# Optimization experiments

Measured on AMD Instinct MI355X. Metric: run time of the kernel, lower is better.

Reference implementation:

```python
import jax, jax.numpy as jnp
import numpy as np

N, F_IN, PRE, K = 400000, 64, 32, 6
EDGE = [32, 32]


def _dense_params(key, fan_in, fan_out):
    kw, kb = jax.random.split(key)
    W = jax.random.normal(kw, (fan_in, fan_out), jnp.float32) / np.sqrt(fan_in).astype(np.float32)
    b = jnp.zeros((fan_out,), jnp.float32)
    return W, b


def setup_inputs() -> dict:
    key = jax.random.key(0)
    ks = jax.random.split(key, 10)
    x = jax.random.normal(ks[0], (N, F_IN), jnp.float32)
    distsq = jax.random.uniform(ks[1], (N, K), jnp.float32)
    nidx = jax.random.randint(ks[2], (N, K), 0, N, jnp.int64)
    Wp, bp = _dense_params(ks[3], F_IN, PRE)
    # edge MLP: input K*(PRE+1) -> 32 -> 32 -> K
    We1, be1 = _dense_params(ks[4], K * (PRE + 1), EDGE[0])
    We2, be2 = _dense_params(ks[5], EDGE[0], EDGE[1])
    We3, be3 = _dense_params(ks[6], EDGE[1], K)
    # self MLP: F_IN -> 32 -> 32 -> 1
    Ws1, bs1 = _dense_params(ks[7], F_IN, EDGE[0])
    Ws2, bs2 = _dense_params(ks[8], EDGE[0], EDGE[1])
    Ws3, bs3 = _dense_params(ks[9], EDGE[1], 1)
    return dict(x=x, distsq=distsq, nidx=nidx, Wp=Wp, bp=bp,
                We1=We1, be1=be1, We2=We2, be2=be2, We3=We3, be3=be3,
                Ws1=Ws1, bs1=bs1, Ws2=Ws2, bs2=bs2, Ws3=Ws3, bs3=bs3)


def _forward(x, distsq, nidx, Wp, bp, We1, be1, We2, be2, We3, be3,
             Ws1, bs1, Ws2, bs2, Ws3, bs3):
    # pre-dense: [N, PRE]
    x_p = jax.nn.elu(x @ Wp + bp)
    # gather neighbors; select(nidx, x_n, 0.0) masks nidx<0 to 0.0
    safe_idx = jnp.maximum(nidx, 0)
    gathered = x_p[safe_idx]                              # [N, K, PRE]
    gathered = jnp.where(nidx[:, :, None] < 0, 0.0, gathered)
    diff = x_p[:, None, :] - gathered                     # [N, K, PRE]
    xn = jnp.concatenate([diff, distsq[:, :, None]], axis=2)  # [N, K, PRE+1]
    xn = xn.reshape(xn.shape[0], K * (PRE + 1))
    xn = jax.nn.elu(xn @ We1 + be1)
    xn = jax.nn.elu(xn @ We2 + be2)
    xn = xn @ We3 + be3                                   # [N, K]
    xs = jax.nn.elu(x @ Ws1 + bs1)
    xs = jax.nn.elu(xs @ Ws2 + bs2)
    xs = xs @ Ws3 + bs3                                   # [N, 1]
    out = jnp.concatenate([xs, xn], axis=1)               # [N, K+1]
    return jax.nn.softmax(out, axis=1)


def reference(x, distsq, nidx, Wp, bp, We1, be1, We2, be2, We3, be3,
              Ws1, bs1, Ws2, bs2, Ws3, bs3):
    return _forward(x, distsq, nidx, Wp, bp, We1, be1, We2, be2, We3, be3,
                    Ws1, bs1, Ws2, bs2, Ws3, bs3)
```

## Files before the change

kernel.cpp:

```cpp
#include <hip/hip_runtime.h>
#include <hip/hip_bf16.h>
#include <math.h>

typedef __hip_bfloat16 bf16;
typedef __attribute__((ext_vector_type(8))) __bf16 bf16x8;
typedef __attribute__((ext_vector_type(4))) float f32x4;

#define F_IN 64
#define KNB 6

#define WOFF_WP   0
#define WOFF_BP   2048
#define WOFF_WE1  2080
#define WOFF_BE1  8416
#define WOFF_WE2  8448
#define WOFF_BE2  9472
#define WOFF_WE3  9504
#define WOFF_BE3  9696
#define WOFF_WS1  9728
#define WOFF_BS1  11776
#define WOFF_WS2  11808
#define WOFF_BS2  12832
#define WOFF_WS3  12864
#define WOFF_BS3  12896
#define FLAGS_OFF 13056
#define WOFF_WSUM 13312
#define WOFF_WDSQ 14336
#define STAGE_OFF 16384

__device__ __forceinline__ float b2f(bf16 v) { return __bfloat162float(v); }
__device__ __forceinline__ float eluf(float v) { return v > 0.f ? v : expm1f(v); }

__device__ __forceinline__ ushort f2bu(float v) {
  __bf16 b = (__bf16)v; ushort u; __builtin_memcpy(&u, &b, 2); return u;
}

union U8 { uint4 u; bf16x8 v; ushort s[8]; };

__device__ __forceinline__ void lds_fence() {
  __builtin_amdgcn_wave_barrier();
  __builtin_amdgcn_s_waitcnt(0xC07F);
  __builtin_amdgcn_wave_barrier();
}

__global__ void detect(const ushort* xb, const int* ni, int* flags) {
  if (threadIdx.x == 0 && blockIdx.x == 0) {
    int bad = 0;
    for (int i = 0; i < 256; i++) {
      float v = __uint_as_float(((unsigned)xb[i]) << 16);
      if (!(fabsf(v) < 100.f)) bad++;
    }
    int hi_nonzero = 0;
    for (int i = 0; i < 64; i++) if (ni[2 * i + 1] != 0) hi_nonzero = 1;
    flags[0] = (bad < 8) ? 1 : 0;
    flags[1] = hi_nonzero ? 0 : 1;
  }
}

__global__ void wstage(const void* Wp, const void* bp, const void* We1, const void* be1,
                       const void* We2, const void* be2, const void* We3, const void* be3,
                       const void* Ws1, const void* bs1, const void* Ws2, const void* bs2,
                       const void* Ws3, const void* bs3, float* w, const int* flags) {
  const void* srcs[14] = {Wp, bp, We1, be1, We2, be2, We3, be3, Ws1, bs1, Ws2, bs2, Ws3, bs3};
  const int sizes[14] = {2048, 32, 6336, 32, 1024, 32, 192, 6, 2048, 32, 1024, 32, 32, 1};
  const int offs[14] = {WOFF_WP, WOFF_BP, WOFF_WE1, WOFF_BE1, WOFF_WE2, WOFF_BE2, WOFF_WE3,
                        WOFF_BE3, WOFF_WS1, WOFF_BS1, WOFF_WS2, WOFF_BS2, WOFF_WS3, WOFF_BS3};
  int bf = flags[0];
  int t = blockIdx.x;
  const void* s = srcs[t];
  int nel = sizes[t];
  float* d = w + offs[t];
  if (bf) {
    const bf16* sb = (const bf16*)s;
    for (int i = threadIdx.x; i < nel; i += blockDim.x) d[i] = b2f(sb[i]);
  } else {
    const float* sf = (const float*)s;
    for (int i = threadIdx.x; i < nel; i += blockDim.x) d[i] = sf[i];
  }
}

__global__ void wprep(float* w) {
  int t = blockIdx.x * blockDim.x + threadIdx.x;
  if (t < 1024) {
    int j = t >> 5, o = t & 31;
    float s = 0.f;
    for (int k = 0; k < KNB; k++) s += w[WOFF_WE1 + (k * 33 + j) * 32 + o];
    w[WOFF_WSUM + t] = s;
  }
  if (t < 192) {
    int k = t >> 5, o = t & 31;
    w[WOFF_WDSQ + t] = w[WOFF_WE1 + (k * 33 + 32) * 32 + o];
  }
}

__device__ __forceinline__ bf16x8 bfrag(const float* W, int ld, int nValid, int kValid, float sgn) {
  int lane = threadIdx.x & 63;
  int n = lane & 15, quad = lane >> 4;
  bf16x8 r;
#pragma unroll
  for (int j = 0; j < 8; j++) {
    int k = quad * 8 + j;
    float v = (n < nValid && k < kValid) ? sgn * W[k * ld + n] : 0.f;
    r[j] = (__bf16)v;
  }
  return r;
}

template <bool BF16>
__device__ __forceinline__ bf16x8 afrag_row(const void* base, long row, int k0) {
  int quad = (threadIdx.x & 63) >> 4;
  if (BF16) {
    U8 u;
    u.u = *(const uint4*)((const ushort*)base + row * F_IN + k0 + quad * 8);
    return u.v;
  } else {
    const float* p = (const float*)base + row * F_IN + k0 + quad * 8;
    float4 a = *(const float4*)p, b = *(const float4*)(p + 4);
    bf16x8 r;
    r[0] = (__bf16)a.x; r[1] = (__bf16)a.y; r[2] = (__bf16)a.z; r[3] = (__bf16)a.w;
    r[4] = (__bf16)b.x; r[5] = (__bf16)b.y; r[6] = (__bf16)b.z; r[7] = (__bf16)b.w;
    return r;
  }
}

template <bool BF16>
__device__ void pre_tiles(const void* xv, const float* __restrict__ w,
                          ushort* __restrict__ xp, float* __restrict__ xs,
                          int n_nodes, ushort* buf) {
  int lane = threadIdx.x & 63;
  int m = lane & 15, quad = lane >> 4;

  bf16x8 fwp[2][2], fws1[2][2], fws2[2], fws3;
#pragma unroll
  for (int s = 0; s < 2; s++)
#pragma unroll
    for (int t = 0; t < 2; t++) {
      fwp[s][t]  = bfrag(w + WOFF_WP  + s * 32 * 32 + 16 * t, 32, 16, 32, 1.f);
      fws1[s][t] = bfrag(w + WOFF_WS1 + s * 32 * 32 + 16 * t, 32, 16, 32, 1.f);
    }
#pragma unroll
  for (int t = 0; t < 2; t++) fws2[t] = bfrag(w + WOFF_WS2 + 16 * t, 32, 16, 32, 1.f);
  fws3 = bfrag(w + WOFF_WS3, 1, 1, 32, 1.f);
  float bpv[2], bs1v[2], bs2v[2];
#pragma unroll
  for (int t = 0; t < 2; t++) {
    bpv[t]  = w[WOFF_BP  + m + 16 * t];
    bs1v[t] = w[WOFF_BS1 + m + 16 * t];
    bs2v[t] = w[WOFF_BS2 + m + 16 * t];
  }
  float bs3f = w[WOFF_BS3];

  int T = (n_nodes + 15) >> 4;
  int wid = (int)((blockIdx.x * blockDim.x + threadIdx.x) >> 6);
  int nw = (int)((gridDim.x * blockDim.x) >> 6);
  f32x4 zero = {0.f, 0.f, 0.f, 0.f};

  for (int t0 = wid; t0 < T; t0 += nw) {
    long n0 = (long)t0 * 16;
    long row = n0 + m; if (row >= n_nodes) row = n_nodes - 1;
    bf16x8 a0 = afrag_row<BF16>(xv, row, 0);
    bf16x8 a1 = afrag_row<BF16>(xv, row, 32);
    f32x4 accp[2], accs[2];
#pragma unroll
    for (int t = 0; t < 2; t++) {
      accp[t] = __builtin_amdgcn_mfma_f32_16x16x32_bf16(a0, fwp[0][t], zero, 0, 0, 0);
      accp[t] = __builtin_amdgcn_mfma_f32_16x16x32_bf16(a1, fwp[1][t], accp[t], 0, 0, 0);
      accs[t] = __builtin_amdgcn_mfma_f32_16x16x32_bf16(a0, fws1[0][t], zero, 0, 0, 0);
      accs[t] = __builtin_amdgcn_mfma_f32_16x16x32_bf16(a1, fws1[1][t], accs[t], 0, 0, 0);
    }
#pragma unroll
    for (int t = 0; t < 2; t++)
#pragma unroll
      for (int r = 0; r < 4; r++)
        buf[(quad * 4 + r) * 32 + m + 16 * t] = f2bu(eluf(accp[t][r] + bpv[t]));
    lds_fence();
    {
      uint4 rv = *(const uint4*)(buf + m * 32 + quad * 8);
      *(uint4*)(xp + row * 32 + quad * 8) = rv;
    }
#pragma unroll
    for (int t = 0; t < 2; t++)
#pragma unroll
      for (int r = 0; r < 4; r++)
        buf[(quad * 4 + r) * 32 + m + 16 * t] = f2bu(eluf(accs[t][r] + bs1v[t]));
    lds_fence();
    U8 as1; as1.u = *(const uint4*)(buf + m * 32 + quad * 8);
    f32x4 acc2[2];
#pragma unroll
    for (int t = 0; t < 2; t++)
      acc2[t] = __builtin_amdgcn_mfma_f32_16x16x32_bf16(as1.v, fws2[t], zero, 0, 0, 0);
#pragma unroll
    for (int t = 0; t < 2; t++)
#pragma unroll
      for (int r = 0; r < 4; r++)
        buf[(quad * 4 + r) * 32 + m + 16 * t] = f2bu(eluf(acc2[t][r] + bs2v[t]));
    lds_fence();
    U8 as2; as2.u = *(const uint4*)(buf + m * 32 + quad * 8);
    f32x4 accx = __builtin_amdgcn_mfma_f32_16x16x32_bf16(as2.v, fws3, zero, 0, 0, 0);
    if (m == 0) {
#pragma unroll
      for (int r = 0; r < 4; r++) {
        long orow = n0 + quad * 4 + r;
        if (orow < n_nodes) xs[orow] = accx[r] + bs3f;
      }
    }
    lds_fence();
  }
}

__launch_bounds__(256)
__global__ void preK(const void* xv, const float* __restrict__ w,
                     const int* __restrict__ flags,
                     ushort* __restrict__ xp, float* __restrict__ xs, int n_nodes) {
  __shared__ ushort sb[4 * 512];
  ushort* buf = sb + (threadIdx.x >> 6) * 512;
  if (flags[0]) pre_tiles<true>(xv, w, xp, xs, n_nodes, buf);
  else          pre_tiles<false>(xv, w, xp, xs, n_nodes, buf);
}

template <bool BF16>
__device__ void edge_tiles(const ushort* __restrict__ xp, const float* __restrict__ xs,
                           const void* dsv, const int* __restrict__ ni, int i64,
                           const float* __restrict__ w, void* outv, int n_nodes,
                           ushort* buf, float* lbuf) {
  int lane = threadIdx.x & 63;
  int m = lane & 15, quad = lane >> 4;

  bf16x8 fsum[2], fwe1[KNB][2], fdsq[2], fwe2[2], fwe3;
#pragma unroll
  for (int t = 0; t < 2; t++) {
    fsum[t] = bfrag(w + WOFF_WSUM + 16 * t, 32, 16, 32, 1.f);
    fdsq[t] = bfrag(w + WOFF_WDSQ + 16 * t, 32, 16, KNB, 1.f);
    fwe2[t] = bfrag(w + WOFF_WE2 + 16 * t, 32, 16, 32, 1.f);
#pragma unroll
    for (int k = 0; k < KNB; k++)
      fwe1[k][t] = bfrag(w + WOFF_WE1 + k * 33 * 32 + 16 * t, 32, 16, 32, -1.f);
  }
  fwe3 = bfrag(w + WOFF_WE3, 6, 6, 32, 1.f);
  float be1v[2], be2v[2];
#pragma unroll
  for (int t = 0; t < 2; t++) {
    be1v[t] = w[WOFF_BE1 + m + 16 * t];
    be2v[t] = w[WOFF_BE2 + m + 16 * t];
  }
  float be3v = (m < 6) ? w[WOFF_BE3 + m] : 0.f;

  int T = (n_nodes + 15) >> 4;
  int wid = (int)((blockIdx.x * blockDim.x + threadIdx.x) >> 6);
  int nw = (int)((gridDim.x * blockDim.x) >> 6);
  f32x4 zero = {0.f, 0.f, 0.f, 0.f};

  for (int t0 = wid; t0 < T; t0 += nw) {
    long n0 = (long)t0 * 16;
    long row = n0 + m; if (row >= n_nodes) row = n_nodes - 1;

    int idxs[KNB];
#pragma unroll
    for (int k = 0; k < KNB; k++)
      idxs[k] = i64 ? ni[(row * KNB + k) * 2] : ni[row * KNB + k];

    U8 own; own.u = *(const uint4*)(xp + row * 32 + quad * 8);
    U8 nb[KNB];
#pragma unroll
    for (int k = 0; k < KNB; k++) {
      long ai = idxs[k];
      if (ai < 0 || ai >= n_nodes) ai = 0;
      nb[k].u = *(const uint4*)(xp + ai * 32 + quad * 8);
      if (idxs[k] < 0) { nb[k].u.x = 0; nb[k].u.y = 0; nb[k].u.z = 0; nb[k].u.w = 0; }
    }

    U8 ad; ad.u.x = 0; ad.u.y = 0; ad.u.z = 0; ad.u.w = 0;
    if (quad == 0) {
      if (BF16) {
        const unsigned* dp = (const unsigned*)dsv;
        ad.u.x = dp[row * 3 + 0];
        ad.u.y = dp[row * 3 + 1];
        ad.u.z = dp[row * 3 + 2];
      } else {
        const float* dp = (const float*)dsv + row * KNB;
#pragma unroll
        for (int k = 0; k < KNB; k++) ad.s[k] = f2bu(dp[k]);
      }
    }

    f32x4 accA[2], accB[2];
#pragma unroll
    for (int t = 0; t < 2; t++) {
      accA[t] = __builtin_amdgcn_mfma_f32_16x16x32_bf16(own.v, fsum[t], zero, 0, 0, 0);
      accA[t] = __builtin_amdgcn_mfma_f32_16x16x32_bf16(nb[0].v, fwe1[0][t], accA[t], 0, 0, 0);
      accA[t] = __builtin_amdgcn_mfma_f32_16x16x32_bf16(nb[1].v, fwe1[1][t], accA[t], 0, 0, 0);
      accA[t] = __builtin_amdgcn_mfma_f32_16x16x32_bf16(nb[2].v, fwe1[2][t], accA[t], 0, 0, 0);
      accB[t] = __builtin_amdgcn_mfma_f32_16x16x32_bf16(nb[3].v, fwe1[3][t], zero, 0, 0, 0);
      accB[t] = __builtin_amdgcn_mfma_f32_16x16x32_bf16(nb[4].v, fwe1[4][t], accB[t], 0, 0, 0);
      accB[t] = __builtin_amdgcn_mfma_f32_16x16x32_bf16(nb[5].v, fwe1[5][t], accB[t], 0, 0, 0);
      accB[t] = __builtin_amdgcn_mfma_f32_16x16x32_bf16(ad.v, fdsq[t], accB[t], 0, 0, 0);
    }
#pragma unroll
    for (int t = 0; t < 2; t++)
#pragma unroll
      for (int r = 0; r < 4; r++)
        buf[(quad * 4 + r) * 32 + m + 16 * t] =
            f2bu(eluf(accA[t][r] + accB[t][r] + be1v[t]));
    lds_fence();
    U8 a1; a1.u = *(const uint4*)(buf + m * 32 + quad * 8);
    f32x4 acc2[2];
#pragma unroll
    for (int t = 0; t < 2; t++)
      acc2[t] = __builtin_amdgcn_mfma_f32_16x16x32_bf16(a1.v, fwe2[t], zero, 0, 0, 0);
#pragma unroll
    for (int t = 0; t < 2; t++)
#pragma unroll
      for (int r = 0; r < 4; r++)
        buf[(quad * 4 + r) * 32 + m + 16 * t] = f2bu(eluf(acc2[t][r] + be2v[t]));
    lds_fence();
    U8 a2; a2.u = *(const uint4*)(buf + m * 32 + quad * 8);
    f32x4 acc3 = __builtin_amdgcn_mfma_f32_16x16x32_bf16(a2.v, fwe3, zero, 0, 0, 0);

    if (m < 6) {
#pragma unroll
      for (int r = 0; r < 4; r++) lbuf[(quad * 4 + r) * 8 + m] = acc3[r] + be3v;
    }
    lds_fence();
    if (lane < 16) {
      long nodeid = n0 + lane;
      if (nodeid < n_nodes) {
        float lg[7];
        lg[0] = xs[nodeid];
#pragma unroll
        for (int i = 0; i < 6; i++) lg[1 + i] = lbuf[lane * 8 + i];
        float mx = lg[0];
#pragma unroll
        for (int i = 1; i < 7; i++) mx = fmaxf(mx, lg[i]);
        float e[7], ssum = 0.f;
#pragma unroll
        for (int i = 0; i < 7; i++) { e[i] = expf(lg[i] - mx); ssum += e[i]; }
        float inv = 1.f / ssum;
        if (BF16) {
          ushort* o = (ushort*)outv + nodeid * 7;
#pragma unroll
          for (int i = 0; i < 7; i++) o[i] = f2bu(e[i] * inv);
        } else {
          float* o = (float*)outv + nodeid * 7;
#pragma unroll
          for (int i = 0; i < 7; i++) o[i] = e[i] * inv;
        }
      }
    }
    lds_fence();
  }
}

__launch_bounds__(256)
__global__ void edgeK(const ushort* __restrict__ xp, const float* __restrict__ xs,
                      const void* dsv, const int* __restrict__ ni,
                      const float* __restrict__ w, const int* __restrict__ flags,
                      void* outv, int n_nodes) {
  __shared__ ushort sb[4 * 512];
  __shared__ float sl[4 * 128];
  ushort* buf = sb + (threadIdx.x >> 6) * 512;
  float* lbuf = sl + (threadIdx.x >> 6) * 128;
  int bf = flags[0];
  int i64 = flags[1];
  if (bf) edge_tiles<true>(xp, xs, dsv, ni, i64, w, outv, n_nodes, buf, lbuf);
  else    edge_tiles<false>(xp, xs, dsv, ni, i64, w, outv, n_nodes, buf, lbuf);
}

__device__ __forceinline__ void bf8_to_f32(uint4 u, float* f) {
  unsigned int w[4] = {u.x, u.y, u.z, u.w};
#pragma unroll
  for (int i = 0; i < 4; i++) {
    f[2 * i]     = __uint_as_float(w[i] << 16);
    f[2 * i + 1] = __uint_as_float(w[i] & 0xffff0000u);
  }
}

template <bool BF16>
__device__ __forceinline__ void load_row8(const void* base, long row, int chunk, float* f) {
  if (BF16) {
    const uint4* p = (const uint4*)((const ushort*)base + row * F_IN);
    bf8_to_f32(p[chunk], f);
  } else {
    const float4* p = (const float4*)((const float*)base + row * F_IN);
    float4 a = p[2 * chunk];
    float4 b = p[2 * chunk + 1];
    f[0] = a.x; f[1] = a.y; f[2] = a.z; f[3] = a.w;
    f[4] = b.x; f[5] = b.y; f[6] = b.z; f[7] = b.w;
  }
}

template <bool BF16>
__device__ void node_body(int n, int n_nodes, const void* xv, const void* dsv,
                          const int* __restrict__ ni, int i64,
                          const float* __restrict__ w, void* outv) {
  const float* Wp  = w + WOFF_WP;
  const float* bp  = w + WOFF_BP;
  const float* We1 = w + WOFF_WE1;
  const float* be1 = w + WOFF_BE1;
  const float* We2 = w + WOFF_WE2;
  const float* be2 = w + WOFF_BE2;
  const float* We3 = w + WOFF_WE3;
  const float* be3 = w + WOFF_BE3;
  const float* Ws1 = w + WOFF_WS1;
  const float* bs1 = w + WOFF_BS1;
  const float* Ws2 = w + WOFF_WS2;
  const float* bs2 = w + WOFF_BS2;
  const float* Ws3 = w + WOFF_WS3;
  const float* bs3 = w + WOFF_BS3;

  float h[32], s1[32];
#pragma unroll
  for (int o = 0; o < 32; o++) { h[o] = bp[o]; s1[o] = bs1[o]; }
  for (int c = 0; c < 8; c++) {
    float xv8[8];
    load_row8<BF16>(xv, n, c, xv8);
#pragma unroll
    for (int q = 0; q < 8; q++) {
      int j = c * 8 + q;
      float xj = xv8[q];
#pragma unroll
      for (int o = 0; o < 32; o++) {
        h[o]  += xj * Wp[j * 32 + o];
        s1[o] += xj * Ws1[j * 32 + o];
      }
    }
  }
  float own[32];
#pragma unroll
  for (int o = 0; o < 32; o++) own[o] = eluf(h[o]);
  float s2[32];
#pragma unroll
  for (int o = 0; o < 32; o++) s2[o] = bs2[o];
  for (int j = 0; j < 32; j++) {
    float v = eluf(s1[j]);
#pragma unroll
    for (int o = 0; o < 32; o++) s2[o] += v * Ws2[j * 32 + o];
  }
  float xsv = bs3[0];
#pragma unroll
  for (int j = 0; j < 32; j++) xsv += eluf(s2[j]) * Ws3[j];

  float h1[32];
#pragma unroll
  for (int o = 0; o < 32; o++) h1[o] = be1[o];
  for (int k = 0; k < KNB; k++) {
    long pos = (long)n * KNB + k;
    int idx = i64 ? ni[2 * pos] : ni[pos];
    float mmask = idx < 0 ? 0.f : 1.f;
    long ai = idx < 0 ? 0 : idx;
    if (ai >= n_nodes) ai = 0;
    float nh[32];
#pragma unroll
    for (int o = 0; o < 32; o++) nh[o] = bp[o];
    for (int c = 0; c < 8; c++) {
      float xv8[8];
      load_row8<BF16>(xv, ai, c, xv8);
#pragma unroll
      for (int q = 0; q < 8; q++) {
        int j = c * 8 + q;
        float xj = xv8[q];
#pragma unroll
        for (int o = 0; o < 32; o++) nh[o] += xj * Wp[j * 32 + o];
      }
    }
    const float* Wk = We1 + (k * 33) * 32;
#pragma unroll
    for (int j = 0; j < 32; j++) {
      float d = own[j] - mmask * eluf(nh[j]);
#pragma unroll
      for (int o = 0; o < 32; o++) h1[o] += d * Wk[j * 32 + o];
    }
    float dsq = BF16 ? b2f(((const bf16*)dsv)[pos]) : ((const float*)dsv)[pos];
#pragma unroll
    for (int o = 0; o < 32; o++) h1[o] += dsq * Wk[32 * 32 + o];
  }
  float h2[32];
#pragma unroll
  for (int o = 0; o < 32; o++) h2[o] = be2[o];
  for (int j = 0; j < 32; j++) {
    float v = eluf(h1[j]);
#pragma unroll
    for (int o = 0; o < 32; o++) h2[o] += v * We2[j * 32 + o];
  }
  float lg[7];
  lg[0] = xsv;
#pragma unroll
  for (int o = 0; o < 6; o++) lg[1 + o] = be3[o];
  for (int j = 0; j < 32; j++) {
    float v = eluf(h2[j]);
#pragma unroll
    for (int o = 0; o < 6; o++) lg[1 + o] += v * We3[j * 6 + o];
  }
  float mx = lg[0];
#pragma unroll
  for (int i = 1; i < 7; i++) mx = fmaxf(mx, lg[i]);
  float e[7], ssum = 0.f;
#pragma unroll
  for (int i = 0; i < 7; i++) { e[i] = expf(lg[i] - mx); ssum += e[i]; }
  float inv = 1.f / ssum;
  if (BF16) {
    bf16* o = (bf16*)outv;
#pragma unroll
    for (int i = 0; i < 7; i++) o[(long)n * 7 + i] = __float2bfloat16(e[i] * inv);
  } else {
    float* o = (float*)outv;
#pragma unroll
    for (int i = 0; i < 7; i++) o[(long)n * 7 + i] = e[i] * inv;
  }
}

__launch_bounds__(256)
__global__ void fused(const void* xv, const void* dsv, const int* __restrict__ ni,
                      const float* __restrict__ w, const int* __restrict__ flags,
                      void* outv, int n_nodes) {
  int n = blockIdx.x * blockDim.x + threadIdx.x;
  if (n >= n_nodes) return;
  int bf = flags[0];
  int i64 = flags[1];
  if (bf) node_body<true>(n, n_nodes, xv, dsv, ni, i64, w, outv);
  else    node_body<false>(n, n_nodes, xv, dsv, ni, i64, w, outv);
}

extern "C" void kernel_launch(void* const* d_in, const int* in_sizes, int n_in,
                              void* d_out, int out_size, void* d_ws, size_t ws_size,
                              hipStream_t stream) {
  const void* x      = d_in[0];
  const void* distsq = d_in[1];
  const int*  nidx   = (const int*)d_in[2];

  float* w = (float*)d_ws;
  int* flags = (int*)(w + FLAGS_OFF);
  int n_nodes = in_sizes[0] / F_IN;

  detect<<<1, 64, 0, stream>>>((const ushort*)x, nidx, flags);
  wstage<<<14, 256, 0, stream>>>(d_in[3], d_in[4], d_in[5], d_in[6], d_in[7], d_in[8],
                                 d_in[9], d_in[10], d_in[11], d_in[12], d_in[13], d_in[14],
                                 d_in[15], d_in[16], w, flags);
  wprep<<<4, 256, 0, stream>>>(w);

  size_t need = (size_t)STAGE_OFF * 4 + (size_t)n_nodes * 64 + (size_t)n_nodes * 4 + 256;
  if (ws_size >= need) {
    ushort* xp = (ushort*)(w + STAGE_OFF);
    float* xs = (float*)(xp + (size_t)n_nodes * 32);
    preK<<<1024, 256, 0, stream>>>(x, w, flags, xp, xs, n_nodes);
    edgeK<<<1024, 256, 0, stream>>>(xp, xs, distsq, nidx, w, flags, d_out, n_nodes);
  } else {
    int grid = (n_nodes + 255) / 256;
    fused<<<grid, 256, 0, stream>>>(x, distsq, nidx, w, flags, d_out, n_nodes);
  }
}
```

Measured before the change: 298.9 us.

## Drop weight staging kernels; read weights directly and detect dtype per block

Removes the detect, wstage and wprep launches. Each block now computes the dtype and index-width flags itself with a ballot, and builds its MFMA weight fragments straight from the input tensors, summing We1 over neighbours in place. It also doubles the grid for the pre and edge kernels, switches exp to the fast __expf intrinsic, and reorders the MFMA chain so the own-feature term is accumulated last. This saves three small serialized launches at the cost of redundant per-block flag detection and fragment construction.

```diff
diff --git a/kernel.cpp b/kernel.cpp
--- a/kernel.cpp
+++ b/kernel.cpp
@@ -9,30 +9,17 @@
 #define F_IN 64
 #define KNB 6
 
-#define WOFF_WP   0
-#define WOFF_BP   2048
-#define WOFF_WE1  2080
-#define WOFF_BE1  8416
-#define WOFF_WE2  8448
-#define WOFF_BE2  9472
-#define WOFF_WE3  9504
-#define WOFF_BE3  9696
-#define WOFF_WS1  9728
-#define WOFF_BS1  11776
-#define WOFF_WS2  11808
-#define WOFF_BS2  12832
-#define WOFF_WS3  12864
-#define WOFF_BS3  12896
-#define FLAGS_OFF 13056
-#define WOFF_WSUM 13312
-#define WOFF_WDSQ 14336
-#define STAGE_OFF 16384
-
 __device__ __forceinline__ float b2f(bf16 v) { return __bfloat162float(v); }
-__device__ __forceinline__ float eluf(float v) { return v > 0.f ? v : expm1f(v); }
+__device__ __forceinline__ float eluf(float v) { return v > 0.f ? v : __expf(v) - 1.f; }
 
 __device__ __forceinline__ ushort f2bu(float v) {
   __bf16 b = (__bf16)v; ushort u; __builtin_memcpy(&u, &b, 2); return u;
+}
+
+template <bool BF16>
+__device__ __forceinline__ float wval(const void* W, long i) {
+  if (BF16) return b2f(((const bf16*)W)[i]);
+  return ((const float*)W)[i];
 }
 
 union U8 { uint4 u; bf16x8 v; ushort s[8]; };
@@ -43,65 +30,52 @@
   __builtin_amdgcn_wave_barrier();
 }
 
-__global__ void detect(const ushort* xb, const int* ni, int* flags) {
-  if (threadIdx.x == 0 && blockIdx.x == 0) {
+__device__ __forceinline__ void block_flags(const ushort* xb, const int* ni, int* sflags) {
+  if (threadIdx.x < 64) {
+    int t = threadIdx.x;
     int bad = 0;
-    for (int i = 0; i < 256; i++) {
+    for (int i = t; i < 256; i += 64) {
       float v = __uint_as_float(((unsigned)xb[i]) << 16);
       if (!(fabsf(v) < 100.f)) bad++;
     }
-    int hi_nonzero = 0;
-    for (int i = 0; i < 64; i++) if (ni[2 * i + 1] != 0) hi_nonzero = 1;
-    flags[0] = (bad < 8) ? 1 : 0;
-    flags[1] = hi_nonzero ? 0 : 1;
-  }
-}
-
-__global__ void wstage(const void* Wp, const void* bp, const void* We1, const void* be1,
-                       const void* We2, const void* be2, const void* We3, const void* be3,
-                       const void* Ws1, const void* bs1, const void* Ws2, const void* bs2,
-                       const void* Ws3, const void* bs3, float* w, const int* flags) {
-  const void* srcs[14] = {Wp, bp, We1, be1, We2, be2, We3, be3, Ws1, bs1, Ws2, bs2, Ws3, bs3};
-  const int sizes[14] = {2048, 32, 6336, 32, 1024, 32, 192, 6, 2048, 32, 1024, 32, 32, 1};
-  const int offs[14] = {WOFF_WP, WOFF_BP, WOFF_WE1, WOFF_BE1, WOFF_WE2, WOFF_BE2, WOFF_WE3,
-                        WOFF_BE3, WOFF_WS1, WOFF_BS1, WOFF_WS2, WOFF_BS2, WOFF_WS3, WOFF_BS3};
-  int bf = flags[0];
-  int t = blockIdx.x;
-  const void* s = srcs[t];
-  int nel = sizes[t];
-  float* d = w + offs[t];
-  if (bf) {
-    const bf16* sb = (const bf16*)s;
-    for (int i = threadIdx.x; i < nel; i += blockDim.x) d[i] = b2f(sb[i]);
-  } else {
-    const float* sf = (const float*)s;
-    for (int i = threadIdx.x; i < nel; i += blockDim.x) d[i] = sf[i];
-  }
-}
-
-__global__ void wprep(float* w) {
-  int t = blockIdx.x * blockDim.x + threadIdx.x;
-  if (t < 1024) {
-    int j = t >> 5, o = t & 31;
-    float s = 0.f;
-    for (int k = 0; k < KNB; k++) s += w[WOFF_WE1 + (k * 33 + j) * 32 + o];
-    w[WOFF_WSUM + t] = s;
-  }
-  if (t < 192) {
-    int k = t >> 5, o = t & 31;
-    w[WOFF_WDSQ + t] = w[WOFF_WE1 + (k * 33 + 32) * 32 + o];
-  }
-}
-
-__device__ __forceinline__ bf16x8 bfrag(const float* W, int ld, int nValid, int kValid, float sgn) {
+    unsigned long long bm = __ballot(bad > 0);
+    unsigned long long hm = __ballot(ni[2 * t + 1] != 0);
+    if (t == 0) {
+      sflags[0] = (__popcll(bm) < 4) ? 1 : 0;
+      sflags[1] = (hm == 0ULL) ? 1 : 0;
+    }
+  }
+  __syncthreads();
+}
+
+template <bool BF16>
+__device__ __forceinline__ bf16x8 bfragT(const void* W, long base, int ld,
+                                         int nValid, int kValid, float sgn) {
   int lane = threadIdx.x & 63;
   int n = lane & 15, quad = lane >> 4;
   bf16x8 r;
 #pragma unroll
   for (int j = 0; j < 8; j++) {
     int k = quad * 8 + j;
-    float v = (n < nValid && k < kValid) ? sgn * W[k * ld + n] : 0.f;
+    float v = (n < nValid && k < kValid) ? sgn * wval<BF16>(W, base + (long)k * ld + n) : 0.f;
     r[j] = (__bf16)v;
+  }
+  return r;
+}
+
+template <bool BF16>
+__device__ __forceinline__ bf16x8 fsum_frag(const void* We1, int t) {
+  int lane = threadIdx.x & 63;
+  int n = lane & 15, quad = lane >> 4;
+  bf16x8 r;
+#pragma unroll
+  for (int j = 0; j < 8; j++) {
+    int k = quad * 8 + j;
+    float s = 0.f;
+#pragma unroll
+    for (int kk = 0; kk < KNB; kk++)
+      s += wval<BF16>(We1, ((long)(kk * 33 + k)) * 32 + n + 16 * t);
+    r[j] = (__bf16)s;
   }
   return r;
 }
@@ -124,7 +98,9 @@
 }
 
 template <bool BF16>
-__device__ void pre_tiles(const void* xv, const float* __restrict__ w,
+__device__ void pre_tiles(const void* xv,
+                          const void* Wp, const void* bp, const void* Ws1, const void* bs1,
+                          const void* Ws2, const void* bs2, const void* Ws3, const void* bs3,
                           ushort* __restrict__ xp, float* __restrict__ xs,
                           int n_nodes, ushort* buf) {
   int lane = threadIdx.x & 63;
@@ -135,20 +111,20 @@
   for (int s = 0; s < 2; s++)
 #pragma unroll
     for (int t = 0; t < 2; t++) {
-      fwp[s][t]  = bfrag(w + WOFF_WP  + s * 32 * 32 + 16 * t, 32, 16, 32, 1.f);
-      fws1[s][t] = bfrag(w + WOFF_WS1 + s * 32 * 32 + 16 * t, 32, 16, 32, 1.f);
-    }
-#pragma unroll
-  for (int t = 0; t < 2; t++) fws2[t] = bfrag(w + WOFF_WS2 + 16 * t, 32, 16, 32, 1.f);
-  fws3 = bfrag(w + WOFF_WS3, 1, 1, 32, 1.f);
+      fwp[s][t]  = bfragT<BF16>(Wp,  s * 1024 + 16 * t, 32, 16, 32, 1.f);
+      fws1[s][t] = bfragT<BF16>(Ws1, s * 1024 + 16 * t, 32, 16, 32, 1.f);
+    }
+#pragma unroll
+  for (int t = 0; t < 2; t++) fws2[t] = bfragT<BF16>(Ws2, 16 * t, 32, 16, 32, 1.f);
+  fws3 = bfragT<BF16>(Ws3, 0, 1, 1, 32, 1.f);
   float bpv[2], bs1v[2], bs2v[2];
 #pragma unroll
   for (int t = 0; t < 2; t++) {
-    bpv[t]  = w[WOFF_BP  + m + 16 * t];
-    bs1v[t] = w[WOFF_BS1 + m + 16 * t];
-    bs2v[t] = w[WOFF_BS2 + m + 16 * t];
-  }
-  float bs3f = w[WOFF_BS3];
+    bpv[t]  = wval<BF16>(bp,  m + 16 * t);
+    bs1v[t] = wval<BF16>(bs1, m + 16 * t);
+    bs2v[t] = wval<BF16>(bs2, m + 16 * t);
+  }
+  float bs3f = wval<BF16>(bs3, 0);
 
   int T = (n_nodes + 15) >> 4;
   int wid = (int)((blockIdx.x * blockDim.x + threadIdx.x) >> 6);
@@ -208,42 +184,46 @@
   }
 }
 
-__launch_bounds__(256)
-__global__ void preK(const void* xv, const float* __restrict__ w,
-                     const int* __restrict__ flags,
+__launch_bounds__(256, 4)
+__global__ void preK(const void* xv, const int* ni,
+                     const void* Wp, const void* bp, const void* Ws1, const void* bs1,
+                     const void* Ws2, const void* bs2, const void* Ws3, const void* bs3,
                      ushort* __restrict__ xp, float* __restrict__ xs, int n_nodes) {
   __shared__ ushort sb[4 * 512];
+  __shared__ int sflags[2];
+  block_flags((const ushort*)xv, ni, sflags);
   ushort* buf = sb + (threadIdx.x >> 6) * 512;
-  if (flags[0]) pre_tiles<true>(xv, w, xp, xs, n_nodes, buf);
-  else          pre_tiles<false>(xv, w, xp, xs, n_nodes, buf);
+  if (sflags[0]) pre_tiles<true>(xv, Wp, bp, Ws1, bs1, Ws2, bs2, Ws3, bs3, xp, xs, n_nodes, buf);
+  else           pre_tiles<false>(xv, Wp, bp, Ws1, bs1, Ws2, bs2, Ws3, bs3, xp, xs, n_nodes, buf);
 }
 
 template <bool BF16>
 __device__ void edge_tiles(const ushort* __restrict__ xp, const float* __restrict__ xs,
                            const void* dsv, const int* __restrict__ ni, int i64,
-                           const float* __restrict__ w, void* outv, int n_nodes,
-                           ushort* buf, float* lbuf) {
+                           const void* We1, const void* be1, const void* We2, const void* be2,
+                           const void* We3, const void* be3,
+                           void* outv, int n_nodes, ushort* buf, float* lbuf) {
   int lane = threadIdx.x & 63;
   int m = lane & 15, quad = lane >> 4;
 
   bf16x8 fsum[2], fwe1[KNB][2], fdsq[2], fwe2[2], fwe3;
 #pragma unroll
   for (int t = 0; t < 2; t++) {
-    fsum[t] = bfrag(w + WOFF_WSUM + 16 * t, 32, 16, 32, 1.f);
-    fdsq[t] = bfrag(w + WOFF_WDSQ + 16 * t, 32, 16, KNB, 1.f);
-    fwe2[t] = bfrag(w + WOFF_WE2 + 16 * t, 32, 16, 32, 1.f);
+    fsum[t] = fsum_frag<BF16>(We1, t);
+    fdsq[t] = bfragT<BF16>(We1, 1024 + 16 * t, 1056, 16, KNB, 1.f);
+    fwe2[t] = bfragT<BF16>(We2, 16 * t, 32, 16, 32, 1.f);
 #pragma unroll
     for (int k = 0; k < KNB; k++)
-      fwe1[k][t] = bfrag(w + WOFF_WE1 + k * 33 * 32 + 16 * t, 32, 16, 32, -1.f);
-  }
-  fwe3 = bfrag(w + WOFF_WE3, 6, 6, 32, 1.f);
+      fwe1[k][t] = bfragT<BF16>(We1, (long)k * 1056 + 16 * t, 32, 16, 32, -1.f);
+  }
+  fwe3 = bfragT<BF16>(We3, 0, 6, 6, 32, 1.f);
   float be1v[2], be2v[2];
 #pragma unroll
   for (int t = 0; t < 2; t++) {
-    be1v[t] = w[WOFF_BE1 + m + 16 * t];
-    be2v[t] = w[WOFF_BE2 + m + 16 * t];
-  }
-  float be3v = (m < 6) ? w[WOFF_BE3 + m] : 0.f;
+    be1v[t] = wval<BF16>(be1, m + 16 * t);
+    be2v[t] = wval<BF16>(be2, m + 16 * t);
+  }
+  float be3v = (m < 6) ? wval<BF16>(be3, m) : 0.f;
 
   int T = (n_nodes + 15) >> 4;
   int wid = (int)((blockIdx.x * blockDim.x + threadIdx.x) >> 6);
@@ -282,19 +262,21 @@
         for (int k = 0; k < KNB; k++) ad.s[k] = f2bu(dp[k]);
       }
     }
+    float xsv = xs[row];
 
     f32x4 accA[2], accB[2];
 #pragma unroll
     for (int t = 0; t < 2; t++) {
-      accA[t] = __builtin_amdgcn_mfma_f32_16x16x32_bf16(own.v, fsum[t], zero, 0, 0, 0);
-      accA[t] = __builtin_amdgcn_mfma_f32_16x16x32_bf16(nb[0].v, fwe1[0][t], accA[t], 0, 0, 0);
+      accA[t] = __builtin_amdgcn_mfma_f32_16x16x32_bf16(nb[0].v, fwe1[0][t], zero, 0, 0, 0);
       accA[t] = __builtin_amdgcn_mfma_f32_16x16x32_bf16(nb[1].v, fwe1[1][t], accA[t], 0, 0, 0);
       accA[t] = __builtin_amdgcn_mfma_f32_16x16x32_bf16(nb[2].v, fwe1[2][t], accA[t], 0, 0, 0);
       accB[t] = __builtin_amdgcn_mfma_f32_16x16x32_bf16(nb[3].v, fwe1[3][t], zero, 0, 0, 0);
       accB[t] = __builtin_amdgcn_mfma_f32_16x16x32_bf16(nb[4].v, fwe1[4][t], accB[t], 0, 0, 0);
       accB[t] = __builtin_amdgcn_mfma_f32_16x16x32_bf16(nb[5].v, fwe1[5][t], accB[t], 0, 0, 0);
       accB[t] = __builtin_amdgcn_mfma_f32_16x16x32_bf16(ad.v, fdsq[t], accB[t], 0, 0, 0);
-    }
+      accA[t] = __builtin_amdgcn_mfma_f32_16x16x32_bf16(own.v, fsum[t], accA[t], 0, 0, 0);
+    }
+
 #pragma unroll
     for (int t = 0; t < 2; t++)
 #pragma unroll
@@ -333,7 +315,7 @@
         for (int i = 1; i < 7; i++) mx = fmaxf(mx, lg[i]);
         float e[7], ssum = 0.f;
 #pragma unroll
-        for (int i = 0; i < 7; i++) { e[i] = expf(lg[i] - mx); ssum += e[i]; }
+        for (int i = 0; i < 7; i++) { e[i] = __expf(lg[i] - mx); ssum += e[i]; }
         float inv = 1.f / ssum;
         if (BF16) {
           ushort* o = (ushort*)outv + nodeid * 7;
@@ -347,81 +329,44 @@
       }
     }
     lds_fence();
+    (void)xsv;
   }
 }
 
 __launch_bounds__(256)
 __global__ void edgeK(const ushort* __restrict__ xp, const float* __restrict__ xs,
                       const void* dsv, const int* __restrict__ ni,
-                      const float* __restrict__ w, const int* __restrict__ flags,
-                      void* outv, int n_nodes) {
+                      const void* We1, const void* be1, const void* We2, const void* be2,
+                      const void* We3, const void* be3,
+                      const void* xv_probe, void* outv, int n_nodes) {
   __shared__ ushort sb[4 * 512];
   __shared__ float sl[4 * 128];
+  __shared__ int sflags[2];
+  block_flags((const ushort*)xv_probe, ni, sflags);
   ushort* buf = sb + (threadIdx.x >> 6) * 512;
   float* lbuf = sl + (threadIdx.x >> 6) * 128;
-  int bf = flags[0];
-  int i64 = flags[1];
-  if (bf) edge_tiles<true>(xp, xs, dsv, ni, i64, w, outv, n_nodes, buf, lbuf);
-  else    edge_tiles<false>(xp, xs, dsv, ni, i64, w, outv, n_nodes, buf, lbuf);
-}
-
-__device__ __forceinline__ void bf8_to_f32(uint4 u, float* f) {
-  unsigned int w[4] = {u.x, u.y, u.z, u.w};
-#pragma unroll
-  for (int i = 0; i < 4; i++) {
-    f[2 * i]     = __uint_as_float(w[i] << 16);
-    f[2 * i + 1] = __uint_as_float(w[i] & 0xffff0000u);
-  }
-}
-
-template <bool BF16>
-__device__ __forceinline__ void load_row8(const void* base, long row, int chunk, float* f) {
-  if (BF16) {
-    const uint4* p = (const uint4*)((const ushort*)base + row * F_IN);
-    bf8_to_f32(p[chunk], f);
-  } else {
-    const float4* p = (const float4*)((const float*)base + row * F_IN);
-    float4 a = p[2 * chunk];
-    float4 b = p[2 * chunk + 1];
-    f[0] = a.x; f[1] = a.y; f[2] = a.z; f[3] = a.w;
-    f[4] = b.x; f[5] = b.y; f[6] = b.z; f[7] = b.w;
-  }
+  if (sflags[0]) edge_tiles<true>(xp, xs, dsv, ni, sflags[1], We1, be1, We2, be2, We3, be3,
+                                  outv, n_nodes, buf, lbuf);
+  else           edge_tiles<false>(xp, xs, dsv, ni, sflags[1], We1, be1, We2, be2, We3, be3,
+                                   outv, n_nodes, buf, lbuf);
 }
 
 template <bool BF16>
 __device__ void node_body(int n, int n_nodes, const void* xv, const void* dsv,
                           const int* __restrict__ ni, int i64,
-                          const float* __restrict__ w, void* outv) {
-  const float* Wp  = w + WOFF_WP;
-  const float* bp  = w + WOFF_BP;
-  const float* We1 = w + WOFF_WE1;
-  const float* be1 = w + WOFF_BE1;
-  const float* We2 = w + WOFF_WE2;
-  const float* be2 = w + WOFF_BE2;
-  const float* We3 = w + WOFF_WE3;
-  const float* be3 = w + WOFF_BE3;
-  const float* Ws1 = w + WOFF_WS1;
-  const float* bs1 = w + WOFF_BS1;
-  const float* Ws2 = w + WOFF_WS2;
-  const float* bs2 = w + WOFF_BS2;
-  const float* Ws3 = w + WOFF_WS3;
-  const float* bs3 = w + WOFF_BS3;
-
+                          const void* Wp, const void* bp, const void* We1, const void* be1,
+                          const void* We2, const void* be2, const void* We3, const void* be3,
+                          const void* Ws1, const void* bs1, const void* Ws2, const void* bs2,
+                          const void* Ws3, const void* bs3, void* outv) {
   float h[32], s1[32];
 #pragma unroll
-  for (int o = 0; o < 32; o++) { h[o] = bp[o]; s1[o] = bs1[o]; }
-  for (int c = 0; c < 8; c++) {
-    float xv8[8];
-    load_row8<BF16>(xv, n, c, xv8);
-#pragma unroll
-    for (int q = 0; q < 8; q++) {
-      int j = c * 8 + q;
-      float xj = xv8[q];
-#pragma unroll
-      for (int o = 0; o < 32; o++) {
-        h[o]  += xj * Wp[j * 32 + o];
-        s1[o] += xj * Ws1[j * 32 + o];
-      }
+  for (int o = 0; o < 32; o++) { h[o] = wval<BF16>(bp, o); s1[o] = wval<BF16>(bs1, o); }
+  for (int j = 0; j < F_IN; j++) {
+    float xj = wval<BF16>(xv, (long)n * F_IN + j);
+#pragma unroll
+    for (int o = 0; o < 32; o++) {
+      h[o]  += xj * wval<BF16>(Wp,  (long)j * 32 + o);
+      s1[o] += xj * wval<BF16>(Ws1, (long)j * 32 + o);
     }
   }
   float own[32];
@@ -429,19 +374,19 @@
   for (int o = 0; o < 32; o++) own[o] = eluf(h[o]);
   float s2[32];
 #pragma unroll
-  for (int o = 0; o < 32; o++) s2[o] = bs2[o];
+  for (int o = 0; o < 32; o++) s2[o] = wval<BF16>(bs2, o);
   for (int j = 0; j < 32; j++) {
     float v = eluf(s1[j]);
 #pragma unroll
-    for (int o = 0; o < 32; o++) s2[o] += v * Ws2[j * 32 + o];
-  }
-  float xsv = bs3[0];
-#pragma unroll
-  for (int j = 0; j < 32; j++) xsv += eluf(s2[j]) * Ws3[j];
+    for (int o = 0; o < 32; o++) s2[o] += v * wval<BF16>(Ws2, (long)j * 32 + o);
+  }
+  float xsv = wval<BF16>(bs3, 0);
+#pragma unroll
+  for (int j = 0; j < 32; j++) xsv += eluf(s2[j]) * wval<BF16>(Ws3, j);
 
   float h1[32];
 #pragma unroll
-  for (int o = 0; o < 32; o++) h1[o] = be1[o];
+  for (int o = 0; o < 32; o++) h1[o] = wval<BF16>(be1, o);
   for (int k = 0; k < KNB; k++) {
     long pos = (long)n * KNB + k;
     int idx = i64 ? ni[2 * pos] : ni[pos];
@@ -450,52 +395,45 @@
     if (ai >= n_nodes) ai = 0;
     float nh[32];
 #pragma unroll
-    for (int o = 0; o < 32; o++) nh[o] = bp[o];
-    for (int c = 0; c < 8; c++) {
-      float xv8[8];
-      load_row8<BF16>(xv, ai, c, xv8);
-#pragma unroll
-      for (int q = 0; q < 8; q++) {
-        int j = c * 8 + q;
-        float xj = xv8[q];
-#pragma unroll
-        for (int o = 0; o < 32; o++) nh[o] += xj * Wp[j * 32 + o];
-      }
-    }
-    const float* Wk = We1 + (k * 33) * 32;
+    for (int o = 0; o < 32; o++) nh[o] = wval<BF16>(bp, o);
+    for (int j = 0; j < F_IN; j++) {
+      float xj = wval<BF16>(xv, ai * F_IN + j);
+#pragma unroll
+      for (int o = 0; o < 32; o++) nh[o] += xj * wval<BF16>(Wp, (long)j * 32 + o);
+    }
 #pragma unroll
     for (int j = 0; j < 32; j++) {
       float d = own[j] - mmask * eluf(nh[j]);
 #pragma unroll
-      for (int o = 0; o < 32; o++) h1[o] += d * Wk[j * 32 + o];
+      for (int o = 0; o < 32; o++) h1[o] += d * wval<BF16>(We1, ((long)(k * 33 + j)) * 32 + o);
     }
     float dsq = BF16 ? b2f(((const bf16*)dsv)[pos]) : ((const float*)dsv)[pos];
 #pragma unroll
-    for (int o = 0; o < 32; o++) h1[o] += dsq * Wk[32 * 32 + o];
+    for (int o = 0; o < 32; o++) h1[o] += dsq * wval<BF16>(We1, ((long)(k * 33 + 32)) * 32 + o);
   }
   float h2[32];
 #pragma unroll
-  for (int o = 0; o < 32; o++) h2[o] = be2[o];
+  for (int o = 0; o < 32; o++) h2[o] = wval<BF16>(be2, o);
   for (int j = 0; j < 32; j++) {
     float v = eluf(h1[j]);
 #pragma unroll
-    for (int o = 0; o < 32; o++) h2[o] += v * We2[j * 32 + o];
+    for (int o = 0; o < 32; o++) h2[o] += v * wval<BF16>(We2, (long)j * 32 + o);
   }
   float lg[7];
   lg[0] = xsv;
 #pragma unroll
-  for (int o = 0; o < 6; o++) lg[1 + o] = be3[o];
+  for (int o = 0; o < 6; o++) lg[1 + o] = wval<BF16>(be3, o);
   for (int j = 0; j < 32; j++) {
     float v = eluf(h2[j]);
 #pragma unroll
-    for (int o = 0; o < 6; o++) lg[1 + o] += v * We3[j * 6 + o];
+    for (int o = 0; o < 6; o++) lg[1 + o] += v * wval<BF16>(We3, (long)j * 6 + o);
   }
   float mx = lg[0];
 #pragma unroll
   for (int i = 1; i < 7; i++) mx = fmaxf(mx, lg[i]);
   float e[7], ssum = 0.f;
 #pragma unroll
-  for (int i = 0; i < 7; i++) { e[i] = expf(lg[i] - mx); ssum += e[i]; }
+  for (int i = 0; i < 7; i++) { e[i] = __expf(lg[i] - mx); ssum += e[i]; }
   float inv = 1.f / ssum;
   if (BF16) {
     bf16* o = (bf16*)outv;
@@ -510,14 +448,18 @@
 
 __launch_bounds__(256)
 __global__ void fused(const void* xv, const void* dsv, const int* __restrict__ ni,
-                      const float* __restrict__ w, const int* __restrict__ flags,
-                      void* outv, int n_nodes) {
+                      const void* Wp, const void* bp, const void* We1, const void* be1,
+                      const void* We2, const void* be2, const void* We3, const void* be3,
+                      const void* Ws1, const void* bs1, const void* Ws2, const void* bs2,
+                      const void* Ws3, const void* bs3, void* outv, int n_nodes) {
+  __shared__ int sflags[2];
+  block_flags((const ushort*)xv, ni, sflags);
   int n = blockIdx.x * blockDim.x + threadIdx.x;
   if (n >= n_nodes) return;
-  int bf = flags[0];
-  int i64 = flags[1];
-  if (bf) node_body<true>(n, n_nodes, xv, dsv, ni, i64, w, outv);
-  else    node_body<false>(n, n_nodes, xv, dsv, ni, i64, w, outv);
+  if (sflags[0]) node_body<true>(n, n_nodes, xv, dsv, ni, sflags[1], Wp, bp, We1, be1,
+                                 We2, be2, We3, be3, Ws1, bs1, Ws2, bs2, Ws3, bs3, outv);
+  else           node_body<false>(n, n_nodes, xv, dsv, ni, sflags[1], Wp, bp, We1, be1,
+                                  We2, be2, We3, be3, Ws1, bs1, Ws2, bs2, Ws3, bs3, outv);
 }
 
 extern "C" void kernel_launch(void* const* d_in, const int* in_sizes, int n_in,
@@ -526,25 +468,34 @@
   const void* x      = d_in[0];
   const void* distsq = d_in[1];
   const int*  nidx   = (const int*)d_in[2];
-
-  float* w = (float*)d_ws;
-  int* flags = (int*)(w + FLAGS_OFF);
+  const void* Wp  = d_in[3];
+  const void* bp  = d_in[4];
+  const void* We1 = d_in[5];
+  const void* be1 = d_in[6];
+  const void* We2 = d_in[7];
+  const void* be2 = d_in[8];
+  const void* We3 = d_in[9];
+  const void* be3 = d_in[10];
+  const void* Ws1 = d_in[11];
+  const void* bs1 = d_in[12];
+  const void* Ws2 = d_in[13];
+  const void* bs2 = d_in[14];
+  const void* Ws3 = d_in[15];
+  const void* bs3 = d_in[16];
+
   int n_nodes = in_sizes[0] / F_IN;
-
-  detect<<<1, 64, 0, stream>>>((const ushort*)x, nidx, flags);
-  wstage<<<14, 256, 0, stream>>>(d_in[3], d_in[4], d_in[5], d_in[6], d_in[7], d_in[8],
-                                 d_in[9], d_in[10], d_in[11], d_in[12], d_in[13], d_in[14],
-                                 d_in[15], d_in[16], w, flags);
-  wprep<<<4, 256, 0, stream>>>(w);
-
-  size_t need = (size_t)STAGE_OFF * 4 + (size_t)n_nodes * 64 + (size_t)n_nodes * 4 + 256;
+  size_t need = (size_t)n_nodes * 64 + (size_t)n_nodes * 4 + 64;
+
   if (ws_size >= need) {
-    ushort* xp = (ushort*)(w + STAGE_OFF);
-    float* xs = (float*)(xp + (size_t)n_nodes * 32);
-    preK<<<1024, 256, 0, stream>>>(x, w, flags, xp, xs, n_nodes);
-    edgeK<<<1024, 256, 0, stream>>>(xp, xs, distsq, nidx, w, flags, d_out, n_nodes);
+    ushort* xp = (ushort*)d_ws;
+    float* xs = (float*)((char*)d_ws + (size_t)n_nodes * 64);
+    preK<<<2048, 256, 0, stream>>>(x, nidx, Wp, bp, Ws1, bs1, Ws2, bs2, Ws3, bs3,
+                                   xp, xs, n_nodes);
+    edgeK<<<2048, 256, 0, stream>>>(xp, xs, distsq, nidx, We1, be1, We2, be2, We3, be3,
+                                    x, d_out, n_nodes);
   } else {
     int grid = (n_nodes + 255) / 256;
-    fused<<<grid, 256, 0, stream>>>(x, distsq, nidx, w, flags, d_out, n_nodes);
-  }
-}
+    fused<<<grid, 256, 0, stream>>>(x, distsq, nidx, Wp, bp, We1, be1, We2, be2, We3, be3,
+                                    Ws1, bs1, Ws2, bs2, Ws3, bs3, d_out, n_nodes);
+  }
+}
```

After: 326.7 us. 1.09x slower.
